# Kernel optimization log

Hardware: AMD Instinct MI355X
Metric: run time of the kernel (lower is better)

Reference implementation:

```python
import jax, jax.numpy as jnp
import numpy as np

HID = 128
FEAT = 16            # glob_in//(2+n_history) = (node_in-1)//4 = (edge_in-1)//4
N_GRAPHS = 512
N_NODES = 100000
N_EDGES = 400000
N_PER = 100000       # effects per branch (glob/node/edge)
A_TOTAL = 300000     # G.num_effects.sum()
EFF_PER_ACT = 4
NUM_ACTIONS = A_TOTAL // EFF_PER_ACT  # 75000 segments (static for jit)


def _lin(k, fan_in, fan_out):
    kw, kb = jax.random.split(k)
    s = 1.0 / np.sqrt(fan_in)
    W = jax.random.uniform(kw, (fan_in, fan_out), jnp.float32, -s, s)
    b = jax.random.uniform(kb, (fan_out,), jnp.float32, -s, s)
    return W, b


def setup_inputs() -> dict:
    key = jax.random.key(0)
    ks = jax.random.split(key, 16)
    globs = jax.random.normal(ks[0], (N_GRAPHS, HID), jnp.float32)
    nodes = jax.random.normal(ks[1], (N_NODES, HID), jnp.float32)
    edges = jax.random.normal(ks[2], (N_EDGES, HID), jnp.float32)
    action_globs = jax.random.normal(ks[3], (N_PER, FEAT), jnp.float32)
    action_nodes = jax.random.normal(ks[4], (N_PER, FEAT), jnp.float32)
    action_edges = jax.random.normal(ks[5], (N_PER, FEAT), jnp.float32)
    row = jax.random.randint(ks[6], (N_EDGES,), 0, N_NODES, jnp.int32)
    col = jax.random.randint(ks[7], (N_EDGES,), 0, N_NODES, jnp.int32)
    U = jax.random.randint(ks[8], (N_PER,), 0, N_GRAPHS, jnp.int32)
    V = jax.random.randint(ks[9], (N_PER,), 0, N_NODES, jnp.int32)
    E = jax.random.randint(ks[10], (N_PER,), 0, N_EDGES, jnp.int32)
    # disjoint write slots in the preallocated actions tensor
    UA = jnp.arange(N_PER, dtype=jnp.int32)
    VA = N_PER + jnp.arange(N_PER, dtype=jnp.int32)
    EA = 2 * N_PER + jnp.arange(N_PER, dtype=jnp.int32)
    # sorted per-effect action ids (4 effects per action)
    actions_batch = (jnp.arange(A_TOTAL, dtype=jnp.int32) // EFF_PER_ACT).astype(jnp.int32)
    glob_W, glob_b = _lin(ks[11], HID + FEAT, HID)
    node_W, node_b = _lin(ks[12], HID + FEAT, HID)
    e1_W, e1_b = _lin(ks[13], 2 * HID + FEAT, HID)
    e2_W, e2_b = _lin(ks[14], 2 * HID, HID)
    pol_W, pol_b = _lin(ks[15], HID, 1)
    return {
        "globs": globs, "nodes": nodes, "edges": edges,
        "action_globs": action_globs, "action_nodes": action_nodes, "action_edges": action_edges,
        "glob_W": glob_W, "glob_b": glob_b, "node_W": node_W, "node_b": node_b,
        "e1_W": e1_W, "e1_b": e1_b, "e2_W": e2_W, "e2_b": e2_b,
        "pol_W": pol_W, "pol_b": pol_b,
        "row": row, "col": col, "U": U, "UA": UA, "V": V, "VA": VA,
        "E": E, "EA": EA, "actions_batch": actions_batch,
    }


def _norm(batch):
    # torch norm(): consecutive group ids starting at batch[0]
    changed = (batch[1:] != batch[:-1]).astype(batch.dtype)
    return batch[0] + jnp.concatenate([jnp.zeros((1,), batch.dtype), jnp.cumsum(changed)])


def reference(globs, nodes, edges, action_globs, action_nodes, action_edges,
              glob_W, glob_b, node_W, node_b, e1_W, e1_b, e2_W, e2_b,
              pol_W, pol_b, row, col, U, UA, V, VA, E, EA, actions_batch):
    actions = jnp.zeros((A_TOTAL, HID), globs.dtype)
    # glob branch: gather globs -> small Linear -> index_put
    ga = jnp.concatenate([globs[U], action_globs], axis=1) @ glob_W + glob_b
    actions = actions.at[UA].set(ga)
    # node branch
    na = jnp.concatenate([nodes[V], action_nodes], axis=1) @ node_W + node_b
    actions = actions.at[VA].set(na)
    # edge branch: two chained Linears over gathered endpoint node feats
    EE = jnp.concatenate([nodes[row[E]], action_edges, nodes[col[E]]], axis=1) @ e1_W + e1_b
    ea = jnp.concatenate([edges[E], EE], axis=1) @ e2_W + e2_b
    actions = actions.at[EA].set(ea)
    # scatter_add segment reduction over action ids
    seg = _norm(actions_batch)
    agg = jax.ops.segment_sum(actions, seg, num_segments=NUM_ACTIONS)  # [NUM_ACTIONS, HID]
    return agg @ pol_W + pol_b  # [NUM_ACTIONS, 1]
```

## Files before the change

kernel.cpp:

```cpp
#include <hip/hip_runtime.h>

#define HID 128
#define FEAT 16
#define N_PER 100000
#define NUM_ACTIONS 75000
#define N_NODES 100000
#define N_GRAPHS 512

#define NSCAL_OFF 1024
#define GSCAL_OFF (NSCAL_OFF + 4 * N_NODES)
#define ESCAL_OFF (GSCAL_OFF + N_GRAPHS)

#define NB 896
#define EB 1120
#define GB 16
#define WORK_BLOCKS (NB + EB + GB)

__device__ __forceinline__ float dot4(float4 a, float4 b) {
    return a.x * b.x + a.y * b.y + a.z * b.z + a.w * b.w;
}

template <int CTRL>
__device__ __forceinline__ float dpp_mov(float x) {
    return __int_as_float(__builtin_amdgcn_update_dpp(
        0, __float_as_int(x), CTRL, 0xF, 0xF, true));
}
__device__ __forceinline__ float red16(float x) {
    x += dpp_mov<0x111>(x);
    x += dpp_mov<0x112>(x);
    x += dpp_mov<0x114>(x);
    x += dpp_mov<0x118>(x);
    return x;
}
__device__ __forceinline__ float red32(float x) {
    x = red16(x);
    x += dpp_mov<0x142>(x);
    return x;
}
__device__ __forceinline__ float red64(float x) {
    x = red32(x);
    x += dpp_mov<0x143>(x);
    return x;
}

__global__ __launch_bounds__(1024) void fold_kernel(
    const float* __restrict__ glob_W, const float* __restrict__ glob_b,
    const float* __restrict__ node_W, const float* __restrict__ node_b,
    const float* __restrict__ e1_W,  const float* __restrict__ e1_b,
    const float* __restrict__ e2_W,  const float* __restrict__ e2_b,
    const float* __restrict__ pol_W, const float* __restrict__ pol_b,
    float* __restrict__ ws)
{
    __shared__ float qEE[HID];
    const int t = threadIdx.x, wave = t >> 6, lane = t & 63;
    const int bid = blockIdx.x;

    const bool needq = (bid >= 26 && bid <= 43);
    if (needq) {
        const int hw = t >> 5, s = t & 31;
        const float4 p4 = *(const float4*)&pol_W[4 * s];
        #pragma unroll
        for (int r = 0; r < 4; ++r) {
            const int k = hw + 32 * r;
            const float4 x = *(const float4*)&e2_W[(HID + k) * HID + 4 * s];
            float acc = red32(dot4(x, p4));
            if (s == 31) qEE[k] = acc;
        }
        __syncthreads();
    }

    const float2 p2 = *(const float2*)&pol_W[2 * lane];
    const int d = bid * 16 + wave;
    if (d == 691) {
        if (lane == 0) ws[691] = pol_b[0];
    } else if (d < 692) {
        float acc;
        if (d < 144) {
            const float2 x = *(const float2*)&glob_W[d * HID + 2 * lane];
            acc = x.x * p2.x + x.y * p2.y;
        } else if (d < 288) {
            const float2 x = *(const float2*)&node_W[(d - 144) * HID + 2 * lane];
            acc = x.x * p2.x + x.y * p2.y;
        } else if (d < 416) {
            const float2 x = *(const float2*)&e2_W[(d - 288) * HID + 2 * lane];
            acc = x.x * p2.x + x.y * p2.y;
        } else if (d < 688) {
            const float2 q2 = *(const float2*)&qEE[2 * lane];
            const float2 x  = *(const float2*)&e1_W[(d - 416) * HID + 2 * lane];
            acc = x.x * q2.x + x.y * q2.y;
        } else if (d == 688) {
            const float2 x = *(const float2*)&glob_b[2 * lane];
            acc = x.x * p2.x + x.y * p2.y;
        } else if (d == 689) {
            const float2 x = *(const float2*)&node_b[2 * lane];
            acc = x.x * p2.x + x.y * p2.y;
        } else {
            const float2 q2 = *(const float2*)&qEE[2 * lane];
            const float2 x1 = *(const float2*)&e1_b[2 * lane];
            const float2 x2 = *(const float2*)&e2_b[2 * lane];
            acc = x1.x * q2.x + x1.y * q2.y + x2.x * p2.x + x2.y * p2.y;
        }
        acc = red64(acc);
        if (lane == 63) ws[d] = acc;
    }
}

__global__ __launch_bounds__(256) void work_kernel(
    const float* __restrict__ nodes, const float* __restrict__ globs,
    const float* __restrict__ edges, const int* __restrict__ E,
    float* __restrict__ ws)
{
    const int t = threadIdx.x, hw = t >> 5, s = t & 31;
    const int bid = blockIdx.x;

    if (bid < NB) {
        const float4 fr = *(const float4*)&ws[416 + 4 * s];
        const float4 fc = *(const float4*)&ws[560 + 4 * s];
        const float4 fn = *(const float4*)&ws[144 + 4 * s];
        for (int h = bid * 8 + hw; h < N_NODES; h += NB * 8) {
            const float4 x = *(const float4*)&nodes[h * HID + 4 * s];
            const float ar = red32(dot4(x, fr));
            const float ac = red32(dot4(x, fc));
            const float az = red32(dot4(x, fn));
            if (s == 31)
                *(float4*)&ws[NSCAL_OFF + 4 * h] = make_float4(ar, ac, az, 0.f);
        }
    } else if (bid < NB + EB) {
        const int eb = bid - NB;
        const float4 q4 = *(const float4*)&ws[288 + 4 * s];
        int g = eb * 8 + hw;
        const int stride = EB * 8;
        int e = (g < N_PER) ? E[g] : 0;
        while (g < N_PER) {
            const int gn = g + stride;
            const int en = (gn < N_PER) ? E[gn] : 0;
            const float4 x = *(const float4*)&edges[e * HID + 4 * s];
            const float acc = red32(dot4(x, q4));
            if (s == 31) ws[ESCAL_OFF + g] = acc;
            g = gn; e = en;
        }
    } else {
        const int gb = bid - NB - EB;
        const float4 g4 = *(const float4*)&ws[4 * s];
        for (int u = gb * 8 + hw; u < N_GRAPHS; u += GB * 8) {
            const float4 x = *(const float4*)&globs[u * HID + 4 * s];
            const float a = red32(dot4(x, g4));
            if (s == 31) ws[GSCAL_OFF + u] = a;
        }
    }
}

__global__ __launch_bounds__(256) void actions_kernel(
    const float* __restrict__ ag, const float* __restrict__ an,
    const float* __restrict__ ae,
    const int* __restrict__ row, const int* __restrict__ col,
    const int* __restrict__ U, const int* __restrict__ V,
    const int* __restrict__ E,
    const float* __restrict__ ws, float* __restrict__ out)
{
    const int tid = threadIdx.x;
    const int qg  = tid >> 4;
    const int ql  = tid & 15;
    const int a   = blockIdx.x * 16 + qg;
    if (a >= NUM_ACTIONS) return;

    float p;
    if (a < 25000) {
        const int gl = 4 * a;
        const float4 f  = *(const float4*)&ag[gl * FEAT + 4 * ql];
        const float4 wf = *(const float4*)&ws[128 + 4 * (ql & 3)];
        p = dot4(f, wf);
        if ((ql & 3) == 0) p += ws[GSCAL_OFF + U[gl + (ql >> 2)]];
        p = red16(p);
        if (ql == 15) out[a] = p + 4.f * ws[688] + ws[691];
    } else if (a < 50000) {
        const int gl = 4 * (a - 25000);
        const float4 f  = *(const float4*)&an[gl * FEAT + 4 * ql];
        const float4 wf = *(const float4*)&ws[272 + 4 * (ql & 3)];
        p = dot4(f, wf);
        if ((ql & 3) == 0) p += ws[NSCAL_OFF + 4 * V[gl + (ql >> 2)] + 2];
        p = red16(p);
        if (ql == 15) out[a] = p + 4.f * ws[689] + ws[691];
    } else {
        const int gl = 4 * (a - 50000);
        const float4 f  = *(const float4*)&ae[gl * FEAT + 4 * ql];
        const float4 wf = *(const float4*)&ws[544 + 4 * (ql & 3)];
        p = dot4(f, wf);
        if (ql < 8) {
            const int e  = E[gl + (ql & 3)];
            const int id = (ql < 4) ? row[e] : col[e];
            p += ws[NSCAL_OFF + 4 * id + ((ql < 4) ? 0 : 1)];
        } else if (ql < 12) {
            p += ws[ESCAL_OFF + gl + (ql - 8)];
        }
        p = red16(p);
        if (ql == 15) out[a] = p + 4.f * ws[690] + ws[691];
    }
}

extern "C" void kernel_launch(void* const* d_in, const int* in_sizes, int n_in,
                              void* d_out, int out_size, void* d_ws, size_t ws_size,
                              hipStream_t stream)
{
    const float* globs  = (const float*)d_in[0];
    const float* nodes  = (const float*)d_in[1];
    const float* edges  = (const float*)d_in[2];
    const float* ag     = (const float*)d_in[3];
    const float* an     = (const float*)d_in[4];
    const float* ae     = (const float*)d_in[5];
    const float* glob_W = (const float*)d_in[6];
    const float* glob_b = (const float*)d_in[7];
    const float* node_W = (const float*)d_in[8];
    const float* node_b = (const float*)d_in[9];
    const float* e1_W   = (const float*)d_in[10];
    const float* e1_b   = (const float*)d_in[11];
    const float* e2_W   = (const float*)d_in[12];
    const float* e2_b   = (const float*)d_in[13];
    const float* pol_W  = (const float*)d_in[14];
    const float* pol_b  = (const float*)d_in[15];
    const int*   row    = (const int*)d_in[16];
    const int*   col    = (const int*)d_in[17];
    const int*   U      = (const int*)d_in[18];
    const int*   V      = (const int*)d_in[20];
    const int*   E      = (const int*)d_in[22];

    float* ws  = (float*)d_ws;
    float* out = (float*)d_out;

    hipLaunchKernelGGL(fold_kernel, dim3(44), dim3(1024), 0, stream,
                       glob_W, glob_b, node_W, node_b, e1_W, e1_b, e2_W, e2_b,
                       pol_W, pol_b, ws);
    hipLaunchKernelGGL(work_kernel, dim3(WORK_BLOCKS), dim3(256), 0, stream,
                       nodes, globs, edges, E, ws);
    hipLaunchKernelGGL(actions_kernel, dim3((NUM_ACTIONS + 15) / 16), dim3(256),
                       0, stream, ag, an, ae, row, col, U, V, E, ws, out);
}
```

Measured before the change: 36.12 us.

## Move action-feature dot products into work kernel, slim final gather kernel

```diff
diff --git a/kernel.cpp b/kernel.cpp
--- a/kernel.cpp
+++ b/kernel.cpp
@@ -10,11 +10,13 @@
 #define NSCAL_OFF 1024
 #define GSCAL_OFF (NSCAL_OFF + 4 * N_NODES)
 #define ESCAL_OFF (GSCAL_OFF + N_GRAPHS)
-
-#define NB 896
-#define EB 1120
+#define PSUM_OFF  (ESCAL_OFF + N_PER)
+
+#define NB 760
+#define EB 968
+#define FB 288
 #define GB 16
-#define WORK_BLOCKS (NB + EB + GB)
+#define WORK_BLOCKS (NB + EB + FB + GB)
 
 __device__ __forceinline__ float dot4(float4 a, float4 b) {
     return a.x * b.x + a.y * b.y + a.z * b.z + a.w * b.w;
@@ -107,8 +109,10 @@
 
 __global__ __launch_bounds__(256) void work_kernel(
     const float* __restrict__ nodes, const float* __restrict__ globs,
-    const float* __restrict__ edges, const int* __restrict__ E,
-    float* __restrict__ ws)
+    const float* __restrict__ edges,
+    const float* __restrict__ ag, const float* __restrict__ an,
+    const float* __restrict__ ae,
+    const int* __restrict__ E, float* __restrict__ ws)
 {
     const int t = threadIdx.x, hw = t >> 5, s = t & 31;
     const int bid = blockIdx.x;
@@ -139,8 +143,21 @@
             if (s == 31) ws[ESCAL_OFF + g] = acc;
             g = gn; e = en;
         }
+    } else if (bid < NB + EB + FB) {
+        const int fb = bid - NB - EB;
+        const int qg = t >> 4, ql = t & 15;
+        for (int a = fb * 16 + qg; a < NUM_ACTIONS; a += FB * 16) {
+            const int br = a / 25000;
+            const int gl = 4 * (a - br * 25000);
+            const float* f = (br == 0) ? ag : (br == 1) ? an : ae;
+            const int fbase = (br == 0) ? 128 : (br == 1) ? 272 : 544;
+            const float4 fv = *(const float4*)&f[gl * FEAT + 4 * ql];
+            const float4 wf = *(const float4*)&ws[fbase + 4 * (ql & 3)];
+            const float p = red16(dot4(fv, wf));
+            if (ql == 15) ws[PSUM_OFF + a] = p;
+        }
     } else {
-        const int gb = bid - NB - EB;
+        const int gb = bid - NB - EB - FB;
         const float4 g4 = *(const float4*)&ws[4 * s];
         for (int u = gb * 8 + hw; u < N_GRAPHS; u += GB * 8) {
             const float4 x = *(const float4*)&globs[u * HID + 4 * s];
@@ -150,51 +167,37 @@
     }
 }
 
-__global__ __launch_bounds__(256) void actions_kernel(
-    const float* __restrict__ ag, const float* __restrict__ an,
-    const float* __restrict__ ae,
+__global__ __launch_bounds__(256) void final_kernel(
     const int* __restrict__ row, const int* __restrict__ col,
     const int* __restrict__ U, const int* __restrict__ V,
     const int* __restrict__ E,
     const float* __restrict__ ws, float* __restrict__ out)
 {
-    const int tid = threadIdx.x;
-    const int qg  = tid >> 4;
-    const int ql  = tid & 15;
-    const int a   = blockIdx.x * 16 + qg;
-    if (a >= NUM_ACTIONS) return;
-
-    float p;
-    if (a < 25000) {
-        const int gl = 4 * a;
-        const float4 f  = *(const float4*)&ag[gl * FEAT + 4 * ql];
-        const float4 wf = *(const float4*)&ws[128 + 4 * (ql & 3)];
-        p = dot4(f, wf);
-        if ((ql & 3) == 0) p += ws[GSCAL_OFF + U[gl + (ql >> 2)]];
-        p = red16(p);
-        if (ql == 15) out[a] = p + 4.f * ws[688] + ws[691];
-    } else if (a < 50000) {
-        const int gl = 4 * (a - 25000);
-        const float4 f  = *(const float4*)&an[gl * FEAT + 4 * ql];
-        const float4 wf = *(const float4*)&ws[272 + 4 * (ql & 3)];
-        p = dot4(f, wf);
-        if ((ql & 3) == 0) p += ws[NSCAL_OFF + 4 * V[gl + (ql >> 2)] + 2];
-        p = red16(p);
-        if (ql == 15) out[a] = p + 4.f * ws[689] + ws[691];
+    const int r = blockIdx.x * 256 + threadIdx.x;
+    if (r >= 3 * N_PER) return;
+    const int br = r / N_PER;
+    const int g  = r - br * N_PER;
+
+    float look, cb;
+    if (br == 0) {
+        look = ws[GSCAL_OFF + U[g]];
+        cb = ws[688];
+    } else if (br == 1) {
+        look = ws[NSCAL_OFF + 4 * V[g] + 2];
+        cb = ws[689];
     } else {
-        const int gl = 4 * (a - 50000);
-        const float4 f  = *(const float4*)&ae[gl * FEAT + 4 * ql];
-        const float4 wf = *(const float4*)&ws[544 + 4 * (ql & 3)];
-        p = dot4(f, wf);
-        if (ql < 8) {
-            const int e  = E[gl + (ql & 3)];
-            const int id = (ql < 4) ? row[e] : col[e];
-            p += ws[NSCAL_OFF + 4 * id + ((ql < 4) ? 0 : 1)];
-        } else if (ql < 12) {
-            p += ws[ESCAL_OFF + gl + (ql - 8)];
-        }
-        p = red16(p);
-        if (ql == 15) out[a] = p + 4.f * ws[690] + ws[691];
+        const int e = E[g];
+        look = ws[ESCAL_OFF + g]
+             + ws[NSCAL_OFF + 4 * row[e] + 0]
+             + ws[NSCAL_OFF + 4 * col[e] + 1];
+        cb = ws[690];
+    }
+    float s4 = look;
+    s4 += dpp_mov<0x111>(s4);
+    s4 += dpp_mov<0x112>(s4);
+    if ((threadIdx.x & 3) == 3) {
+        const int a = r >> 2;
+        out[a] = s4 + ws[PSUM_OFF + a] + 4.f * cb + ws[691];
     }
 }
 
@@ -231,7 +234,7 @@
                        glob_W, glob_b, node_W, node_b, e1_W, e1_b, e2_W, e2_b,
                        pol_W, pol_b, ws);
     hipLaunchKernelGGL(work_kernel, dim3(WORK_BLOCKS), dim3(256), 0, stream,
-                       nodes, globs, edges, E, ws);
-    hipLaunchKernelGGL(actions_kernel, dim3((NUM_ACTIONS + 15) / 16), dim3(256),
-                       0, stream, ag, an, ae, row, col, U, V, E, ws, out);
-}
+                       nodes, globs, edges, ag, an, ae, E, ws);
+    hipLaunchKernelGGL(final_kernel, dim3((3 * N_PER + 255) / 256), dim3(256),
+                       0, stream, row, col, U, V, E, ws, out);
+}
```

Result: no change. 35.68 us (median of 2 runs) (-1.2%).
